# Kernel tuning notes

Measured on AMD Instinct MI355X. Metric: run time of the kernel, lower is better.

Reference implementation:

```python
import jax, jax.numpy as jnp
import numpy as np

K = 128
T_X = 4
DATA_LENGTH = 512
B_GROUPS = 64
B = B_GROUPS * DATA_LENGTH
INV_SQRT2 = 0.7071067811865476  # 1/sqrt(2), haar reconstruction filter coeff


def setup_inputs() -> dict:
    key = jax.random.key(0)
    ks = jax.random.split(key, 9)
    x = jax.random.normal(ks[0], (B, T_X, K), jnp.float32)
    y = jax.random.normal(ks[1], (B, 1, K), jnp.float32)
    s = 1.0 / np.sqrt(K).astype(np.float32)
    Wq = jax.random.normal(ks[2], (K, K), jnp.float32) * s
    Wk = jax.random.normal(ks[3], (K, K), jnp.float32) * s
    Wv = jax.random.normal(ks[4], (K, K), jnp.float32) * s
    conv_w = jax.random.normal(ks[5], (K, 2 * K), jnp.float32) * (1.0 / np.sqrt(2 * K).astype(np.float32))
    conv_b = jax.random.normal(ks[6], (K,), jnp.float32) * 0.01
    bn_gamma = jnp.ones((K,), jnp.float32)
    bn_beta = jnp.zeros((K,), jnp.float32)
    bn_mean = jax.random.normal(ks[7], (K,), jnp.float32) * 0.1
    bn_var = jax.random.uniform(ks[8], (K,), jnp.float32, 0.5, 1.5)
    return dict(x=x, y=y, Wq=Wq, Wk=Wk, Wv=Wv, conv_w=conv_w, conv_b=conv_b,
                bn_gamma=bn_gamma, bn_beta=bn_beta, bn_mean=bn_mean, bn_var=bn_var,
                data_length=DATA_LENGTH)


def _idwt_haar(L, H):
    # inverse 1D haar transform along last dim: (Bg, C, 1, T) -> (Bg, C, 1, 2T)
    even = (L + H) * INV_SQRT2
    odd = (L - H) * INV_SQRT2
    out = jnp.stack([even, odd], axis=-1)  # (..., T, 2)
    return out.reshape(L.shape[:-1] + (L.shape[-1] * 2,))


def reference(x, y, Wq, Wk, Wv, conv_w, conv_b, bn_gamma, bn_beta, bn_mean, bn_var, data_length):
    b, t_x, k = x.shape  # t_x = 4 bands, heads = 1, t_y = 1
    q = jnp.einsum('btk,ok->bto', y, Wq)                      # (b, 1, k)
    keys = jnp.einsum('bsk,ok->bso', x, Wk) * (1.0 / (k ** 0.5))  # (b, 4, k)
    v = jnp.einsum('bsk,ok->bso', x, Wv)                      # (b, 4, k)
    dot = jnp.einsum('bto,bso->bs', q, keys)                  # (b, 4)
    w = jax.nn.softmax(dot, axis=1)                           # softmax over the 4 bands
    outs = w[:, :, None] * v                                  # (b, 4, k) band-weighted values
    Bg = b // data_length
    # per band: (b, k) -> (Bg, dl, 1, k) -> permute -> (Bg, k, 1, dl)
    o = outs.reshape(Bg, data_length, t_x, k).transpose(2, 0, 3, 1)  # (4, Bg, k, dl)
    o = o[:, :, :, None, :]                                   # (4, Bg, k, 1, dl)
    out_L = _idwt_haar(o[0], o[1])                            # (Bg, k, 1, 2*dl)
    out_H = _idwt_haar(o[2], o[3])
    out = jnp.concatenate([out_L, out_H], axis=1)             # (Bg, 2k, 1, 2*dl)
    # transition: 1x1 conv + BN (eval mode) + LeakyReLU(0.01)
    z = jnp.einsum('bcij,oc->boij', out, conv_w) + conv_b[None, :, None, None]
    scale = (bn_gamma * jax.lax.rsqrt(bn_var + 1e-5))[None, :, None, None]
    z = (z - bn_mean[None, :, None, None]) * scale + bn_beta[None, :, None, None]
    return jnp.where(z > 0, z, 0.01 * z)
```

## Files before the change

### kernel.cpp

```cpp
#include <hip/hip_runtime.h>
#include <stdint.h>

typedef __attribute__((ext_vector_type(8))) short bf16x8;
typedef __attribute__((ext_vector_type(4))) float f32x4;

__device__ __forceinline__ unsigned short f2bf(float x) {
    union { float f; uint32_t u; } v; v.f = x;
    uint32_t r = v.u + 0x7FFFu + ((v.u >> 16) & 1u);
    return (unsigned short)(r >> 16);
}
__device__ __forceinline__ uint32_t pack2bf(float a, float b) {
    return (uint32_t)f2bf(a) | ((uint32_t)f2bf(b) << 16);
}
__device__ __forceinline__ float bf2f(uint32_t lo) {
    union { uint32_t u; float f; } v; v.u = lo << 16; return v.f;
}
__device__ __forceinline__ float lrelu(float v) { return v > 0.f ? v : 0.01f * v; }

__global__ __launch_bounds__(256) void precompute_kernel(
    const float* __restrict__ Wq, const float* __restrict__ Wk,
    const float* __restrict__ Wv, const float* __restrict__ conv_w,
    const float* __restrict__ conv_b, const float* __restrict__ bn_gamma,
    const float* __restrict__ bn_beta, const float* __restrict__ bn_mean,
    const float* __restrict__ bn_var,
    unsigned short* __restrict__ Gh, unsigned short* __restrict__ Gl,
    unsigned short* __restrict__ Mh, unsigned short* __restrict__ Ml,
    float* __restrict__ scale2, float* __restrict__ bias2)
{
    __shared__ float lds0[2176];
    __shared__ float lds1[2176];
    const int tid = threadIdx.x;
    const int bid = blockIdx.x;

    if (bid == 192) {
        if (tid < 128) {
            float sc = bn_gamma[tid] * rsqrtf(bn_var[tid] + 1e-5f);
            scale2[tid] = sc;
            bias2[tid]  = (conv_b[tid] - bn_mean[tid]) * sc + bn_beta[tid];
        }
        return;
    }

    if (bid < 64) {
        int i0 = (bid >> 3) << 4, j0 = (bid & 7) << 4;
        #pragma unroll
        for (int t = 0; t < 8; ++t) {
            int e = tid + t * 256;
            int o = e >> 4, c = e & 15;
            lds0[o * 17 + c] = Wk[o * 128 + i0 + c];
            lds1[o * 17 + c] = Wq[o * 128 + j0 + c];
        }
        __syncthreads();
        int ti = tid >> 4, tj = tid & 15;
        float sum = 0.f;
        #pragma unroll 8
        for (int o = 0; o < 128; ++o) sum += lds0[o * 17 + ti] * lds1[o * 17 + tj];
        float val = sum * 0.08838834764831845f;
        unsigned short h = f2bf(val);
        int idx = (i0 + ti) * 128 + j0 + tj;
        Gh[idx] = h;
        Gl[idx] = f2bf(val - bf2f(h));
    } else {
        int rel = bid - 64;
        int o0 = (rel >> 4) << 4, c0 = (rel & 15) << 4;
        int cw0 = (c0 >> 7) << 7, cc0 = c0 & 127;
        #pragma unroll
        for (int t = 0; t < 8; ++t) {
            int e = tid + t * 256;
            int to = e >> 7, k = e & 127;
            lds0[to * 132 + k] = conv_w[(o0 + to) * 256 + cw0 + k];
            int kk = e >> 4, c = e & 15;
            lds1[kk * 17 + c] = Wv[kk * 128 + cc0 + c];
        }
        __syncthreads();
        int to = tid >> 4, tc = tid & 15;
        float sum = 0.f;
        #pragma unroll 8
        for (int k = 0; k < 128; ++k) sum += lds0[to * 132 + k] * lds1[k * 17 + tc];
        float val = sum * 0.7071067811865476f;
        unsigned short h = f2bf(val);
        int idx = (o0 + to) * 256 + c0 + tc;
        Mh[idx] = h;
        Ml[idx] = f2bf(val - bf2f(h));
    }
}

#define UADDR(row, lane) (((row) << 8) + (((((lane) >> 2) ^ ((row) & 7))) << 4) + ((((lane) << 2)) & 15))
#define AADDR(row, gi)   (((row) << 8) + ((((gi) ^ ((row) & 7))) << 4))

__global__ __launch_bounds__(256) void fused_kernel(
    const float* __restrict__ x, const float* __restrict__ y,
    const unsigned short* __restrict__ Gh, const unsigned short* __restrict__ Gl,
    const unsigned short* __restrict__ Mh, const unsigned short* __restrict__ Ml,
    const float* __restrict__ scale2, const float* __restrict__ bias2,
    float* __restrict__ out)
{
    __shared__ __align__(16) unsigned char smem[32768];
    float* gbufF = (float*)(smem + 16384);

    const int tid = threadIdx.x;
    const int w = tid >> 6;
    const int l = tid & 63;
    const int quad = l >> 4;
    const int bid = blockIdx.x;
    const int b0 = bid * 32;

    {
        const float* yb = y + (size_t)b0 * 128;
        #pragma unroll
        for (int it = 0; it < 4; ++it) {
            int idx = tid + it * 256;
            int row = idx >> 5, q = idx & 31;
            float4 v = *(const float4*)(yb + row * 128 + q * 4);
            *(float4*)(smem + row * 512 + ((q ^ (row & 7)) << 4)) = v;
        }
    }
    __syncthreads();

    {
        f32x4 accg[2][2];
        #pragma unroll
        for (int rt = 0; rt < 2; ++rt)
            #pragma unroll
            for (int n = 0; n < 2; ++n) accg[rt][n] = (f32x4){0.f, 0.f, 0.f, 0.f};
        #pragma unroll
        for (int ks = 0; ks < 4; ++ks) {
            int ksr = (ks + bid) & 3;
            union { bf16x8 v; unsigned short u[8]; } Ah[2], Al[2];
            #pragma unroll
            for (int rt = 0; rt < 2; ++rt) {
                int yrow = 16 * rt + (l & 15);
                int g0 = ksr * 8 + quad * 2;
                float4 v0 = *(const float4*)(smem + yrow * 512 + (((g0 + 0) ^ (yrow & 7)) << 4));
                float4 v1 = *(const float4*)(smem + yrow * 512 + (((g0 + 1) ^ (yrow & 7)) << 4));
                float f[8] = {v0.x, v0.y, v0.z, v0.w, v1.x, v1.y, v1.z, v1.w};
                #pragma unroll
                for (int j = 0; j < 8; ++j) {
                    unsigned short h = f2bf(f[j]);
                    Ah[rt].u[j] = h;
                    Al[rt].u[j] = f2bf(f[j] - bf2f(h));
                }
            }
            #pragma unroll
            for (int n = 0; n < 2; ++n) {
                int nt = 2 * w + n;
                int off = (nt * 16 + (l & 15)) * 128 + ksr * 32 + quad * 8;
                bf16x8 bh = *(const bf16x8*)(Gh + off);
                bf16x8 bl = *(const bf16x8*)(Gl + off);
                #pragma unroll
                for (int rt = 0; rt < 2; ++rt) {
                    accg[rt][n] = __builtin_amdgcn_mfma_f32_16x16x32_bf16(Ah[rt].v, bh, accg[rt][n], 0, 0, 0);
                    accg[rt][n] = __builtin_amdgcn_mfma_f32_16x16x32_bf16(Al[rt].v, bh, accg[rt][n], 0, 0, 0);
                    accg[rt][n] = __builtin_amdgcn_mfma_f32_16x16x32_bf16(Ah[rt].v, bl, accg[rt][n], 0, 0, 0);
                }
            }
        }
        #pragma unroll
        for (int n = 0; n < 2; ++n) {
            int i = (2 * w + n) * 16 + (l & 15);
            #pragma unroll
            for (int rt = 0; rt < 2; ++rt)
                #pragma unroll
                for (int r = 0; r < 4; ++r)
                    gbufF[(16 * rt + quad * 4 + r) * 128 + i] = accg[rt][n][r];
        }
    }
    __syncthreads();

    #pragma unroll 4
    for (int s = 0; s < 8; ++s) {
        int b_loc = 8 * w + s;
        const float2* xb = (const float2*)(x + (size_t)(b0 + b_loc) * 512);
        float2 x0 = xb[l], x1 = xb[64 + l], x2 = xb[128 + l], x3 = xb[192 + l];
        float2 g2 = *(const float2*)(gbufF + b_loc * 128 + 2 * l);
        float p0 = x0.x * g2.x + x0.y * g2.y;
        float p1 = x1.x * g2.x + x1.y * g2.y;
        float p2 = x2.x * g2.x + x2.y * g2.y;
        float p3 = x3.x * g2.x + x3.y * g2.y;
        #pragma unroll
        for (int off = 32; off >= 1; off >>= 1) {
            p0 += __shfl_xor(p0, off);
            p1 += __shfl_xor(p1, off);
            p2 += __shfl_xor(p2, off);
            p3 += __shfl_xor(p3, off);
        }
        float mx = fmaxf(fmaxf(p0, p1), fmaxf(p2, p3));
        float e0 = __expf(p0 - mx), e1 = __expf(p1 - mx);
        float e2 = __expf(p2 - mx), e3 = __expf(p3 - mx);
        float inv = 1.f / (e0 + e1 + e2 + e3);
        float w0 = e0 * inv, w1 = e1 * inv, w2 = e2 * inv, w3 = e3 * inv;
        int r0 = 2 * b_loc, r1 = r0 + 1;
        *(uint32_t*)(smem + UADDR(r0, l)) = pack2bf(w0 * x0.x + w1 * x1.x, w0 * x0.y + w1 * x1.y);
        *(uint32_t*)(smem + UADDR(r1, l)) = pack2bf(w0 * x0.x - w1 * x1.x, w0 * x0.y - w1 * x1.y);
        *(uint32_t*)(smem + 16384 + UADDR(r0, l)) = pack2bf(w2 * x2.x + w3 * x3.x, w2 * x2.y + w3 * x3.y);
        *(uint32_t*)(smem + 16384 + UADDR(r1, l)) = pack2bf(w2 * x2.x - w3 * x3.x, w2 * x2.y - w3 * x3.y);
    }
    __syncthreads();

    f32x4 acc[4][2];
    #pragma unroll
    for (int rb = 0; rb < 4; ++rb)
        #pragma unroll
        for (int n = 0; n < 2; ++n) acc[rb][n] = (f32x4){0.f, 0.f, 0.f, 0.f};

    #pragma unroll
    for (int ks = 0; ks < 8; ++ks) {
        int ksr = (ks + bid) & 7;
        int half = ksr >> 2, kk = ksr & 3;
        int base = half << 14;
        int gi = kk * 4 + quad;
        bf16x8 a[4];
        #pragma unroll
        for (int rb = 0; rb < 4; ++rb)
            a[rb] = *(const bf16x8*)(smem + base + AADDR(16 * rb + (l & 15), gi));
        #pragma unroll
        for (int n = 0; n < 2; ++n) {
            int off = ((2 * w + n) * 16 + (l & 15)) * 256 + half * 128 + kk * 32 + quad * 8;
            bf16x8 bh = *(const bf16x8*)(Mh + off);
            bf16x8 bl = *(const bf16x8*)(Ml + off);
            #pragma unroll
            for (int rb = 0; rb < 4; ++rb) {
                acc[rb][n] = __builtin_amdgcn_mfma_f32_16x16x32_bf16(a[rb], bh, acc[rb][n], 0, 0, 0);
                acc[rb][n] = __builtin_amdgcn_mfma_f32_16x16x32_bf16(a[rb], bl, acc[rb][n], 0, 0, 0);
            }
        }
    }

    {
        float* outp = out + (size_t)(bid >> 4) * 131072 + (bid & 15) * 64;
        #pragma unroll
        for (int n = 0; n < 2; ++n) {
            int o = (2 * w + n) * 16 + (l & 15);
            float sc = scale2[o], bi = bias2[o];
            #pragma unroll
            for (int rb = 0; rb < 4; ++rb) {
                int jb = 16 * rb + quad * 4;
                f32x4 a = acc[rb][n];
                float4 r;
                r.x = lrelu(a[0] * sc + bi);
                r.y = lrelu(a[1] * sc + bi);
                r.z = lrelu(a[2] * sc + bi);
                r.w = lrelu(a[3] * sc + bi);
                *(float4*)(outp + (size_t)o * 1024 + jb) = r;
            }
        }
    }
}

extern "C" void kernel_launch(void* const* d_in, const int* in_sizes, int n_in,
                              void* d_out, int out_size, void* d_ws, size_t ws_size,
                              hipStream_t stream)
{
    (void)in_sizes; (void)n_in; (void)out_size; (void)ws_size;
    const float* x        = (const float*)d_in[0];
    const float* y        = (const float*)d_in[1];
    const float* Wq       = (const float*)d_in[2];
    const float* Wk       = (const float*)d_in[3];
    const float* Wv       = (const float*)d_in[4];
    const float* conv_w   = (const float*)d_in[5];
    const float* conv_b   = (const float*)d_in[6];
    const float* bn_gamma = (const float*)d_in[7];
    const float* bn_beta  = (const float*)d_in[8];
    const float* bn_mean  = (const float*)d_in[9];
    const float* bn_var   = (const float*)d_in[10];

    unsigned char* ws = (unsigned char*)d_ws;
    unsigned short* Gh = (unsigned short*)(ws);
    unsigned short* Gl = (unsigned short*)(ws + 32768);
    unsigned short* Mh = (unsigned short*)(ws + 65536);
    unsigned short* Ml = (unsigned short*)(ws + 131072);
    float* scale2      = (float*)(ws + 196608);
    float* bias2       = (float*)(ws + 197120);

    hipLaunchKernelGGL(precompute_kernel, dim3(193), dim3(256), 0, stream,
                       Wq, Wk, Wv, conv_w, conv_b, bn_gamma, bn_beta, bn_mean,
                       bn_var, Gh, Gl, Mh, Ml, scale2, bias2);
    hipLaunchKernelGGL(fused_kernel, dim3(1024), dim3(256), 0, stream,
                       x, y, Gh, Gl, Mh, Ml, scale2, bias2, (float*)d_out);
}
```

Measured before the change: 154.3 us.

## Pre-split y to bf16 hi/lo in LDS, widen x loads, prefetch first weight tiles

```diff
diff --git a/kernel.cpp b/kernel.cpp
--- a/kernel.cpp
+++ b/kernel.cpp
@@ -85,7 +85,6 @@
     }
 }
 
-#define UADDR(row, lane) (((row) << 8) + (((((lane) >> 2) ^ ((row) & 7))) << 4) + ((((lane) << 2)) & 15))
 #define AADDR(row, gi)   (((row) << 8) + ((((gi) ^ ((row) & 7))) << 4))
 
 __global__ __launch_bounds__(256) void fused_kernel(
@@ -102,17 +101,39 @@
     const int w = tid >> 6;
     const int l = tid & 63;
     const int quad = l >> 4;
+    const int i16 = l & 15;
     const int bid = blockIdx.x;
     const int b0 = bid * 32;
 
+    const int ks0 = bid & 3;
+    bf16x8 pgh[2], pgl[2];
+    #pragma unroll
+    for (int n = 0; n < 2; ++n) {
+        int off = ((2 * w + n) * 16 + i16) * 128 + ks0 * 32 + quad * 8;
+        pgh[n] = *(const bf16x8*)(Gh + off);
+        pgl[n] = *(const bf16x8*)(Gl + off);
+    }
+
     {
         const float* yb = y + (size_t)b0 * 128;
         #pragma unroll
-        for (int it = 0; it < 4; ++it) {
-            int idx = tid + it * 256;
-            int row = idx >> 5, q = idx & 31;
-            float4 v = *(const float4*)(yb + row * 128 + q * 4);
-            *(float4*)(smem + row * 512 + ((q ^ (row & 7)) << 4)) = v;
+        for (int it = 0; it < 2; ++it) {
+            int j = tid + it * 256;
+            int row = j >> 4, gk = j & 15;
+            float4 v0 = *(const float4*)(yb + row * 128 + gk * 8);
+            float4 v1 = *(const float4*)(yb + row * 128 + gk * 8 + 4);
+            float f[8] = {v0.x, v0.y, v0.z, v0.w, v1.x, v1.y, v1.z, v1.w};
+            uint32_t hi[4], lo[4];
+            #pragma unroll
+            for (int e = 0; e < 4; ++e) {
+                unsigned short h0 = f2bf(f[2 * e]), h1 = f2bf(f[2 * e + 1]);
+                hi[e] = (uint32_t)h0 | ((uint32_t)h1 << 16);
+                lo[e] = (uint32_t)f2bf(f[2 * e] - bf2f(h0)) |
+                        ((uint32_t)f2bf(f[2 * e + 1] - bf2f(h1)) << 16);
+            }
+            int addr = AADDR(row, gk);
+            *(uint4*)(smem + addr)        = make_uint4(hi[0], hi[1], hi[2], hi[3]);
+            *(uint4*)(smem + 8192 + addr) = make_uint4(lo[0], lo[1], lo[2], lo[3]);
         }
     }
     __syncthreads();
@@ -126,38 +147,34 @@
         #pragma unroll
         for (int ks = 0; ks < 4; ++ks) {
             int ksr = (ks + bid) & 3;
-            union { bf16x8 v; unsigned short u[8]; } Ah[2], Al[2];
+            bf16x8 ah[2], al[2];
             #pragma unroll
             for (int rt = 0; rt < 2; ++rt) {
-                int yrow = 16 * rt + (l & 15);
-                int g0 = ksr * 8 + quad * 2;
-                float4 v0 = *(const float4*)(smem + yrow * 512 + (((g0 + 0) ^ (yrow & 7)) << 4));
-                float4 v1 = *(const float4*)(smem + yrow * 512 + (((g0 + 1) ^ (yrow & 7)) << 4));
-                float f[8] = {v0.x, v0.y, v0.z, v0.w, v1.x, v1.y, v1.z, v1.w};
-                #pragma unroll
-                for (int j = 0; j < 8; ++j) {
-                    unsigned short h = f2bf(f[j]);
-                    Ah[rt].u[j] = h;
-                    Al[rt].u[j] = f2bf(f[j] - bf2f(h));
+                int row = 16 * rt + i16;
+                int addr = AADDR(row, ksr * 4 + quad);
+                ah[rt] = *(const bf16x8*)(smem + addr);
+                al[rt] = *(const bf16x8*)(smem + 8192 + addr);
+            }
+            #pragma unroll
+            for (int n = 0; n < 2; ++n) {
+                bf16x8 bh, bl;
+                if (ks == 0) { bh = pgh[n]; bl = pgl[n]; }
+                else {
+                    int off = ((2 * w + n) * 16 + i16) * 128 + ksr * 32 + quad * 8;
+                    bh = *(const bf16x8*)(Gh + off);
+                    bl = *(const bf16x8*)(Gl + off);
                 }
-            }
-            #pragma unroll
-            for (int n = 0; n < 2; ++n) {
-                int nt = 2 * w + n;
-                int off = (nt * 16 + (l & 15)) * 128 + ksr * 32 + quad * 8;
-                bf16x8 bh = *(const bf16x8*)(Gh + off);
-                bf16x8 bl = *(const bf16x8*)(Gl + off);
                 #pragma unroll
                 for (int rt = 0; rt < 2; ++rt) {
-                    accg[rt][n] = __builtin_amdgcn_mfma_f32_16x16x32_bf16(Ah[rt].v, bh, accg[rt][n], 0, 0, 0);
-                    accg[rt][n] = __builtin_amdgcn_mfma_f32_16x16x32_bf16(Al[rt].v, bh, accg[rt][n], 0, 0, 0);
-                    accg[rt][n] = __builtin_amdgcn_mfma_f32_16x16x32_bf16(Ah[rt].v, bl, accg[rt][n], 0, 0, 0);
+                    accg[rt][n] = __builtin_amdgcn_mfma_f32_16x16x32_bf16(ah[rt], bh, accg[rt][n], 0, 0, 0);
+                    accg[rt][n] = __builtin_amdgcn_mfma_f32_16x16x32_bf16(al[rt], bh, accg[rt][n], 0, 0, 0);
+                    accg[rt][n] = __builtin_amdgcn_mfma_f32_16x16x32_bf16(ah[rt], bl, accg[rt][n], 0, 0, 0);
                 }
             }
         }
         #pragma unroll
         for (int n = 0; n < 2; ++n) {
-            int i = (2 * w + n) * 16 + (l & 15);
+            int i = (2 * w + n) * 16 + i16;
             #pragma unroll
             for (int rt = 0; rt < 2; ++rt)
                 #pragma unroll
@@ -167,33 +184,65 @@
     }
     __syncthreads();
 
-    #pragma unroll 4
-    for (int s = 0; s < 8; ++s) {
-        int b_loc = 8 * w + s;
-        const float2* xb = (const float2*)(x + (size_t)(b0 + b_loc) * 512);
-        float2 x0 = xb[l], x1 = xb[64 + l], x2 = xb[128 + l], x3 = xb[192 + l];
-        float2 g2 = *(const float2*)(gbufF + b_loc * 128 + 2 * l);
-        float p0 = x0.x * g2.x + x0.y * g2.y;
-        float p1 = x1.x * g2.x + x1.y * g2.y;
-        float p2 = x2.x * g2.x + x2.y * g2.y;
-        float p3 = x3.x * g2.x + x3.y * g2.y;
-        #pragma unroll
-        for (int off = 32; off >= 1; off >>= 1) {
-            p0 += __shfl_xor(p0, off);
-            p1 += __shfl_xor(p1, off);
-            p2 += __shfl_xor(p2, off);
-            p3 += __shfl_xor(p3, off);
-        }
-        float mx = fmaxf(fmaxf(p0, p1), fmaxf(p2, p3));
-        float e0 = __expf(p0 - mx), e1 = __expf(p1 - mx);
-        float e2 = __expf(p2 - mx), e3 = __expf(p3 - mx);
+    union F8 { float4 v[2]; float f[8]; };
+    #pragma unroll
+    for (int pass = 0; pass < 2; ++pass) {
+        int b_loc = 8 * w + pass * 4 + quad;
+        const float* xb = x + (size_t)(b0 + b_loc) * 512;
+        F8 X[4];
+        #pragma unroll
+        for (int t = 0; t < 4; ++t) {
+            X[t].v[0] = *(const float4*)(xb + t * 128 + i16 * 8);
+            X[t].v[1] = *(const float4*)(xb + t * 128 + i16 * 8 + 4);
+        }
+        float4 ga = *(const float4*)(gbufF + b_loc * 128 + i16 * 8);
+        float4 gb = *(const float4*)(gbufF + b_loc * 128 + i16 * 8 + 4);
+        float p[4];
+        #pragma unroll
+        for (int t = 0; t < 4; ++t) {
+            float4 a = X[t].v[0], b = X[t].v[1];
+            p[t] = a.x * ga.x + a.y * ga.y + a.z * ga.z + a.w * ga.w
+                 + b.x * gb.x + b.y * gb.y + b.z * gb.z + b.w * gb.w;
+        }
+        #pragma unroll
+        for (int off = 8; off >= 1; off >>= 1) {
+            p[0] += __shfl_xor(p[0], off);
+            p[1] += __shfl_xor(p[1], off);
+            p[2] += __shfl_xor(p[2], off);
+            p[3] += __shfl_xor(p[3], off);
+        }
+        float mx = fmaxf(fmaxf(p[0], p[1]), fmaxf(p[2], p[3]));
+        float e0 = __expf(p[0] - mx), e1 = __expf(p[1] - mx);
+        float e2 = __expf(p[2] - mx), e3 = __expf(p[3] - mx);
         float inv = 1.f / (e0 + e1 + e2 + e3);
         float w0 = e0 * inv, w1 = e1 * inv, w2 = e2 * inv, w3 = e3 * inv;
         int r0 = 2 * b_loc, r1 = r0 + 1;
-        *(uint32_t*)(smem + UADDR(r0, l)) = pack2bf(w0 * x0.x + w1 * x1.x, w0 * x0.y + w1 * x1.y);
-        *(uint32_t*)(smem + UADDR(r1, l)) = pack2bf(w0 * x0.x - w1 * x1.x, w0 * x0.y - w1 * x1.y);
-        *(uint32_t*)(smem + 16384 + UADDR(r0, l)) = pack2bf(w2 * x2.x + w3 * x3.x, w2 * x2.y + w3 * x3.y);
-        *(uint32_t*)(smem + 16384 + UADDR(r1, l)) = pack2bf(w2 * x2.x - w3 * x3.x, w2 * x2.y - w3 * x3.y);
+        int a0 = AADDR(r0, i16), a1 = AADDR(r1, i16);
+        uint32_t eL[4], oL[4], eH[4], oH[4];
+        #pragma unroll
+        for (int e = 0; e < 4; ++e) {
+            int c0 = 2 * e, c1 = 2 * e + 1;
+            eL[e] = pack2bf(w0 * X[0].f[c0] + w1 * X[1].f[c0], w0 * X[0].f[c1] + w1 * X[1].f[c1]);
+            oL[e] = pack2bf(w0 * X[0].f[c0] - w1 * X[1].f[c0], w0 * X[0].f[c1] - w1 * X[1].f[c1]);
+            eH[e] = pack2bf(w2 * X[2].f[c0] + w3 * X[3].f[c0], w2 * X[2].f[c1] + w3 * X[3].f[c1]);
+            oH[e] = pack2bf(w2 * X[2].f[c0] - w3 * X[3].f[c0], w2 * X[2].f[c1] - w3 * X[3].f[c1]);
+        }
+        *(uint4*)(smem + a0)         = make_uint4(eL[0], eL[1], eL[2], eL[3]);
+        *(uint4*)(smem + a1)         = make_uint4(oL[0], oL[1], oL[2], oL[3]);
+        *(uint4*)(smem + 16384 + a0) = make_uint4(eH[0], eH[1], eH[2], eH[3]);
+        *(uint4*)(smem + 16384 + a1) = make_uint4(oH[0], oH[1], oH[2], oH[3]);
+    }
+
+    const int ks0b = bid & 7;
+    bf16x8 pmh[2], pml[2];
+    {
+        int half = ks0b >> 2, kk = ks0b & 3;
+        #pragma unroll
+        for (int n = 0; n < 2; ++n) {
+            int off = ((2 * w + n) * 16 + i16) * 256 + half * 128 + kk * 32 + quad * 8;
+            pmh[n] = *(const bf16x8*)(Mh + off);
+            pml[n] = *(const bf16x8*)(Ml + off);
+        }
     }
     __syncthreads();
 
@@ -212,12 +261,16 @@
         bf16x8 a[4];
         #pragma unroll
         for (int rb = 0; rb < 4; ++rb)
-            a[rb] = *(const bf16x8*)(smem + base + AADDR(16 * rb + (l & 15), gi));
+            a[rb] = *(const bf16x8*)(smem + base + AADDR(16 * rb + i16, gi));
         #pragma unroll
         for (int n = 0; n < 2; ++n) {
-            int off = ((2 * w + n) * 16 + (l & 15)) * 256 + half * 128 + kk * 32 + quad * 8;
-            bf16x8 bh = *(const bf16x8*)(Mh + off);
-            bf16x8 bl = *(const bf16x8*)(Ml + off);
+            bf16x8 bh, bl;
+            if (ks == 0) { bh = pmh[n]; bl = pml[n]; }
+            else {
+                int off = ((2 * w + n) * 16 + i16) * 256 + half * 128 + kk * 32 + quad * 8;
+                bh = *(const bf16x8*)(Mh + off);
+                bl = *(const bf16x8*)(Ml + off);
+            }
             #pragma unroll
             for (int rb = 0; rb < 4; ++rb) {
                 acc[rb][n] = __builtin_amdgcn_mfma_f32_16x16x32_bf16(a[rb], bh, acc[rb][n], 0, 0, 0);
@@ -230,7 +283,7 @@
         float* outp = out + (size_t)(bid >> 4) * 131072 + (bid & 15) * 64;
         #pragma unroll
         for (int n = 0; n < 2; ++n) {
-            int o = (2 * w + n) * 16 + (l & 15);
+            int o = (2 * w + n) * 16 + i16;
             float sc = scale2[o], bi = bias2[o];
             #pragma unroll
             for (int rb = 0; rb < 4; ++rb) {
```

Measured after the change: 154.4 us. About the same (+0.0%).
